# Performance work log

Measured on AMD Instinct MI355X. Metric: run time of the kernel, lower is better.

Reference implementation:

```python
import jax, jax.numpy as jnp
import numpy as np

CH = 512      # input channels
V = 320       # codewords per group
G = 2         # groups
CV_DIM = 256  # codevector_dim (wav2vec2 default)
D = CV_DIM // G
TAU = 2.0     # gumbel temperature


def setup_inputs() -> dict:
    key = jax.random.key(0)
    k1, k2, k3, k4 = jax.random.split(key, 4)
    B, T = 32, 1024
    x = jax.random.normal(k1, (B, T, CH), jnp.float32)
    W_proj = jax.random.normal(k2, (CH, G * V), jnp.float32) / np.sqrt(CH)
    b_proj = jnp.zeros((G * V,), jnp.float32)
    codevectors = jax.random.normal(k3, (G, V, D), jnp.float32) * 0.02
    # uniform noise, transformed to Gumbel inside reference
    u_noise = jax.random.uniform(k4, (B, T, G, V), jnp.float32,
                                 minval=1e-6, maxval=1.0 - 1e-6)
    return {"x": x, "W_proj": W_proj, "b_proj": b_proj,
            "codevectors": codevectors, "u_noise": u_noise}


def reference(x, W_proj, b_proj, codevectors, u_noise):
    B, T, _ = x.shape
    # projection to per-group logits: [B,T,G,V]
    logits = (x @ W_proj + b_proj).reshape(B, T, G, V)
    # gumbel-softmax (hard, straight-through)
    g = -jnp.log(-jnp.log(u_noise))
    soft = jax.nn.softmax((logits + g) / TAU, axis=-1)
    hard = jax.nn.one_hot(jnp.argmax(soft, axis=-1), V, dtype=soft.dtype)
    st = hard + soft - jax.lax.stop_gradient(soft)
    # combine selected codewords per group, concat groups -> [B,T,CV_DIM]
    out = jnp.einsum('btgv,gvd->btgd', st, codevectors).reshape(B, T, G * D)
    return out
```

## Files before the change

kernel.cpp:

```cpp
#include <hip/hip_runtime.h>
#include <cmath>

namespace {

typedef _Float16 half8 __attribute__((ext_vector_type(8)));
typedef _Float16 half4v __attribute__((ext_vector_type(4)));
typedef float f32x4 __attribute__((ext_vector_type(4)));

constexpr int M_TOTAL = 32 * 1024;
constexpr int K_CH    = 512;
constexpr int NV      = 640;
constexpr int D_CV    = 128;
constexpr int NSLOT   = 10;

constexpr int BM = 128, BN = 128, BK = 32;
constexpr int NTILE  = NV / BN;
constexpr int NPANEL = M_TOTAL / BM;
constexpr int NBLK   = NTILE * NPANEL;
constexpr int KT     = K_CH / BK;

constexpr float LO_SCALE = 4096.0f;
constexpr float LO_INV   = 1.0f / 4096.0f;

__device__ __forceinline__ void gld16(const void* g, void* l) {
  __builtin_amdgcn_global_load_lds(
      (__attribute__((address_space(1))) void*)g,
      (__attribute__((address_space(3))) void*)l, 16, 0, 0);
}

__global__ __launch_bounds__(256)
void prep_w(const float* __restrict__ W, _Float16* __restrict__ Wth,
            _Float16* __restrict__ Wtl)
{
  __shared__ float tile[32][33];
  const int bk = blockIdx.x & 15;
  const int bn = blockIdx.x >> 4;
  const int k0 = bk * 32, n0 = bn * 32;
  const int t = threadIdx.x;
  const int nn = t & 31, kk = t >> 5;
  #pragma unroll
  for (int p = 0; p < 4; ++p)
    tile[kk + p * 8][nn] = W[(size_t)(k0 + kk + p * 8) * NV + n0 + nn];
  __syncthreads();
  const int kx = t & 31, nx = t >> 5;
  #pragma unroll
  for (int p = 0; p < 4; ++p) {
    const float v = tile[kx][nx + p * 8];
    const _Float16 h = (_Float16)v;
    const _Float16 l = (_Float16)((v - (float)h) * LO_SCALE);
    const size_t o = (size_t)(n0 + nx + p * 8) * K_CH + k0 + kx;
    Wth[o] = h;
    Wtl[o] = l;
  }
}

__global__ __launch_bounds__(256)
void prep_x(const float* __restrict__ x, _Float16* __restrict__ Xh,
            _Float16* __restrict__ Xl)
{
  const size_t i = ((size_t)blockIdx.x * 256 + threadIdx.x) * 2;
  #pragma unroll
  for (int j = 0; j < 2; ++j) {
    const float4 v = reinterpret_cast<const float4*>(x)[i + j];
    const float* pv = &v.x;
    half4v h, l;
    #pragma unroll
    for (int e = 0; e < 4; ++e) {
      const _Float16 hh = (_Float16)pv[e];
      h[e] = hh;
      l[e] = (_Float16)((pv[e] - (float)hh) * LO_SCALE);
    }
    reinterpret_cast<half4v*>(Xh)[i + j] = h;
    reinterpret_cast<half4v*>(Xl)[i + j] = l;
  }
}

__global__ __launch_bounds__(256, 2)
void gvq_mfma5(const _Float16* __restrict__ Xh, const _Float16* __restrict__ Xl,
               const _Float16* __restrict__ Wth, const _Float16* __restrict__ Wtl,
               const float* __restrict__ bias, const float* __restrict__ u,
               float* __restrict__ pval, int* __restrict__ pidx)
{
  __shared__ __align__(16) _Float16 lds[2][16384];

  const int chunk = NBLK / 8;
  const int nid   = (blockIdx.x % 8) * chunk + blockIdx.x / 8;
  const int panel = nid / NTILE, ntile = nid % NTILE;
  const int m0 = panel * BM, n0 = ntile * BN;

  const int t    = threadIdx.x;
  const int wv   = t >> 6, lane = t & 63;
  const int wr   = wv >> 1, wc = wv & 1;
  const int li   = lane & 15, q = lane >> 4;

  const int r0 = t >> 2;
  const int gc = (t & 3) ^ ((t >> 3) & 3);
  const _Float16* pxh0 = Xh  + (size_t)(m0 + r0) * K_CH + gc * 8;
  const _Float16* pxh1 = Xh  + (size_t)(m0 + 64 + r0) * K_CH + gc * 8;
  const _Float16* pxl0 = Xl  + (size_t)(m0 + r0) * K_CH + gc * 8;
  const _Float16* pxl1 = Xl  + (size_t)(m0 + 64 + r0) * K_CH + gc * 8;
  const _Float16* pbh0 = Wth + (size_t)(n0 + r0) * K_CH + gc * 8;
  const _Float16* pbh1 = Wth + (size_t)(n0 + 64 + r0) * K_CH + gc * 8;
  const _Float16* pbl0 = Wtl + (size_t)(n0 + r0) * K_CH + gc * 8;
  const _Float16* pbl1 = Wtl + (size_t)(n0 + 64 + r0) * K_CH + gc * 8;

  f32x4 acc1[4][4];
  f32x4 acc2[4][4];
  #pragma unroll
  for (int i = 0; i < 4; ++i)
    #pragma unroll
    for (int j = 0; j < 4; ++j) {
      acc1[i][j] = (f32x4){0.f, 0.f, 0.f, 0.f};
      acc2[i][j] = (f32x4){0.f, 0.f, 0.f, 0.f};
    }

  auto stage = [&](int kt, int b) {
    const int ko = kt * BK;
    _Float16* L = &lds[b][0];
    gld16(pxh0 + ko, L + 0     + wv * 512);
    gld16(pxh1 + ko, L + 2048  + wv * 512);
    gld16(pxl0 + ko, L + 4096  + wv * 512);
    gld16(pxl1 + ko, L + 6144  + wv * 512);
    gld16(pbh0 + ko, L + 8192  + wv * 512);
    gld16(pbh1 + ko, L + 10240 + wv * 512);
    gld16(pbl0 + ko, L + 12288 + wv * 512);
    gld16(pbl1 + ko, L + 14336 + wv * 512);
  };

  const int soff = ((q ^ ((li >> 1) & 3)) << 3);
  const int arow = (wr * 64 + li) * 32;
  const int brow = (wc * 64 + li) * 32;

  stage(0, 0);
  stage(1, 1);
  #pragma unroll
  for (int kt = 0; kt < KT; ++kt) {
    const int cur = kt & 1;
    if (kt < KT - 1) asm volatile("s_waitcnt vmcnt(8)" ::: "memory");
    else             asm volatile("s_waitcnt vmcnt(0)" ::: "memory");
    __builtin_amdgcn_s_barrier();

    const _Float16* L = &lds[cur][0];
    half8 ah[4], al[4], bh[4], bl[4];
    #pragma unroll
    for (int f = 0; f < 4; ++f) {
      ah[f] = *reinterpret_cast<const half8*>(L + arow + f * 512 + soff);
      al[f] = *reinterpret_cast<const half8*>(L + 4096  + arow + f * 512 + soff);
      bh[f] = *reinterpret_cast<const half8*>(L + 8192  + brow + f * 512 + soff);
      bl[f] = *reinterpret_cast<const half8*>(L + 12288 + brow + f * 512 + soff);
    }
    asm volatile("s_waitcnt lgkmcnt(0)" ::: "memory");
    __builtin_amdgcn_sched_barrier(0);
    __builtin_amdgcn_s_barrier();

    if (kt + 2 < KT) stage(kt + 2, cur);

    __builtin_amdgcn_s_setprio(1);
    #pragma unroll
    for (int fm = 0; fm < 4; ++fm)
      #pragma unroll
      for (int fn = 0; fn < 4; ++fn) {
        acc1[fm][fn] = __builtin_amdgcn_mfma_f32_16x16x32_f16(
            ah[fm], bh[fn], acc1[fm][fn], 0, 0, 0);
        acc2[fm][fn] = __builtin_amdgcn_mfma_f32_16x16x32_f16(
            ah[fm], bl[fn], acc2[fm][fn], 0, 0, 0);
        acc2[fm][fn] = __builtin_amdgcn_mfma_f32_16x16x32_f16(
            al[fm], bh[fn], acc2[fm][fn], 0, 0, 0);
      }
    __builtin_amdgcn_s_setprio(0);
  }

  const int colbase = n0 + wc * 64 + li;
  float bb[4];
  #pragma unroll
  for (int fn = 0; fn < 4; ++fn) bb[fn] = bias[colbase + fn * 16];

  const int slot = ntile * 2 + wc;
  #pragma unroll
  for (int fm = 0; fm < 4; ++fm) {
    #pragma unroll
    for (int r = 0; r < 4; ++r) {
      const int m = m0 + wr * 64 + fm * 16 + q * 4 + r;
      float bv = -INFINITY;
      int   bi = 0x7fffffff;
      #pragma unroll
      for (int fn = 0; fn < 4; ++fn) {
        const float uu  = u[(size_t)m * NV + colbase + fn * 16];
        const float g   = -__logf(-__logf(uu));
        const float val = acc1[fm][fn][r] + acc2[fm][fn][r] * LO_INV
                          + bb[fn] + g;
        const int   n   = colbase + fn * 16;
        if (val > bv) { bv = val; bi = n; }
      }
      #pragma unroll
      for (int s = 1; s <= 8; s <<= 1) {
        const float ov = __shfl_xor(bv, s);
        const int   oi = __shfl_xor(bi, s);
        if (ov > bv || (ov == bv && oi < bi)) { bv = ov; bi = oi; }
      }
      if (li == 0) {
        pval[(size_t)m * NSLOT + slot] = bv;
        pidx[(size_t)m * NSLOT + slot] = bi;
      }
    }
  }
}

__global__ __launch_bounds__(256)
void gvq_gather(const float* __restrict__ pval,
                const int*   __restrict__ pidx,
                const float* __restrict__ cv,
                float* __restrict__ out)
{
  const int tid  = threadIdx.x;
  const int w    = tid >> 6;
  const int lane = tid & 63;
  const int m    = blockIdx.x * 4 + w;
  const int g    = lane >> 5;

  const float* pv = &pval[(size_t)m * NSLOT + g * 5];
  const int*   pi = &pidx[(size_t)m * NSLOT + g * 5];
  float bv = pv[0];
  int   bi = pi[0];
  #pragma unroll
  for (int s = 1; s < 5; ++s) {
    const float v = pv[s];
    const int   i = pi[s];
    if (v > bv || (v == bv && i < bi)) { bv = v; bi = i; }
  }
  const float4 src = *reinterpret_cast<const float4*>(
      &cv[(size_t)bi * D_CV + (lane & 31) * 4]);
  *reinterpret_cast<float4*>(&out[(size_t)m * 256 + lane * 4]) = src;
}

}

extern "C" void kernel_launch(void* const* d_in, const int* in_sizes, int n_in,
                              void* d_out, int out_size, void* d_ws, size_t ws_size,
                              hipStream_t stream)
{
  const float* x    = (const float*)d_in[0];
  const float* W    = (const float*)d_in[1];
  const float* bias = (const float*)d_in[2];
  const float* cv   = (const float*)d_in[3];
  const float* u    = (const float*)d_in[4];
  float* out = (float*)d_out;

  _Float16* Wth  = (_Float16*)d_ws;
  _Float16* Wtl  = Wth + (size_t)NV * K_CH;
  float*    pval = (float*)(Wtl + (size_t)NV * K_CH);
  int*      pidx = (int*)(pval + (size_t)M_TOTAL * NSLOT);
  _Float16* Xh   = (_Float16*)(pidx + (size_t)M_TOTAL * NSLOT);
  _Float16* Xl   = Xh + (size_t)M_TOTAL * K_CH;

  hipLaunchKernelGGL(prep_w, dim3(320), dim3(256), 0, stream, W, Wth, Wtl);
  hipLaunchKernelGGL(prep_x, dim3(8192), dim3(256), 0, stream, x, Xh, Xl);
  hipLaunchKernelGGL(gvq_mfma5, dim3(NBLK), dim3(256), 0, stream,
                     Xh, Xl, Wth, Wtl, bias, u, pval, pidx);
  hipLaunchKernelGGL(gvq_gather, dim3(M_TOTAL / 4), dim3(256), 0, stream,
                     pval, pidx, cv, out);
}
```

Measured before the change: 132.7 us.

## Shrink GEMM N-tile to 64, re-split waves along M, single-stage prefetch

Halves the block tile width from 128 to 64 columns, so each of the four waves now owns 32 rows by all 64 columns instead of a 2x2 wave grid. LDS per block drops, launch bounds move to 3 blocks per CU, and the pipeline becomes prefetch-next-then-compute with a full vmcnt(0) wait and barrier per k-step. Each block now writes one argmax slot per tile rather than two. The goal is higher occupancy and fewer per-wave accumulators, at the cost of reloading the X panel twice as often across N tiles and less latency hiding per block.

Result: slower. 137.2 us (+3.4%).

```diff
diff --git a/kernel.cpp b/kernel.cpp
--- a/kernel.cpp
+++ b/kernel.cpp
@@ -13,11 +13,13 @@
 constexpr int D_CV    = 128;
 constexpr int NSLOT   = 10;
 
-constexpr int BM = 128, BN = 128, BK = 32;
+constexpr int BM = 128, BN = 64, BK = 32;
 constexpr int NTILE  = NV / BN;
 constexpr int NPANEL = M_TOTAL / BM;
 constexpr int NBLK   = NTILE * NPANEL;
 constexpr int KT     = K_CH / BK;
+
+constexpr int LBUF = 12288;
 
 constexpr float LO_SCALE = 4096.0f;
 constexpr float LO_INV   = 1.0f / 4096.0f;
@@ -75,13 +77,13 @@
   }
 }
 
-__global__ __launch_bounds__(256, 2)
-void gvq_mfma5(const _Float16* __restrict__ Xh, const _Float16* __restrict__ Xl,
+__global__ __launch_bounds__(256, 3)
+void gvq_mfma6(const _Float16* __restrict__ Xh, const _Float16* __restrict__ Xl,
                const _Float16* __restrict__ Wth, const _Float16* __restrict__ Wtl,
                const float* __restrict__ bias, const float* __restrict__ u,
                float* __restrict__ pval, int* __restrict__ pidx)
 {
-  __shared__ __align__(16) _Float16 lds[2][16384];
+  __shared__ __align__(16) _Float16 lds[2 * LBUF];
 
   const int chunk = NBLK / 8;
   const int nid   = (blockIdx.x % 8) * chunk + blockIdx.x / 8;
@@ -90,24 +92,19 @@
 
   const int t    = threadIdx.x;
   const int wv   = t >> 6, lane = t & 63;
-  const int wr   = wv >> 1, wc = wv & 1;
   const int li   = lane & 15, q = lane >> 4;
 
   const int r0 = t >> 2;
   const int gc = (t & 3) ^ ((t >> 3) & 3);
-  const _Float16* pxh0 = Xh  + (size_t)(m0 + r0) * K_CH + gc * 8;
-  const _Float16* pxh1 = Xh  + (size_t)(m0 + 64 + r0) * K_CH + gc * 8;
-  const _Float16* pxl0 = Xl  + (size_t)(m0 + r0) * K_CH + gc * 8;
-  const _Float16* pxl1 = Xl  + (size_t)(m0 + 64 + r0) * K_CH + gc * 8;
-  const _Float16* pbh0 = Wth + (size_t)(n0 + r0) * K_CH + gc * 8;
-  const _Float16* pbh1 = Wth + (size_t)(n0 + 64 + r0) * K_CH + gc * 8;
-  const _Float16* pbl0 = Wtl + (size_t)(n0 + r0) * K_CH + gc * 8;
-  const _Float16* pbl1 = Wtl + (size_t)(n0 + 64 + r0) * K_CH + gc * 8;
-
-  f32x4 acc1[4][4];
-  f32x4 acc2[4][4];
-  #pragma unroll
-  for (int i = 0; i < 4; ++i)
+  const _Float16* pxh = Xh  + (size_t)(m0 + r0) * K_CH + gc * 8;
+  const _Float16* pxl = Xl  + (size_t)(m0 + r0) * K_CH + gc * 8;
+  const _Float16* pbh = Wth + (size_t)(n0 + r0) * K_CH + gc * 8;
+  const _Float16* pbl = Wtl + (size_t)(n0 + r0) * K_CH + gc * 8;
+
+  f32x4 acc1[2][4];
+  f32x4 acc2[2][4];
+  #pragma unroll
+  for (int i = 0; i < 2; ++i)
     #pragma unroll
     for (int j = 0; j < 4; ++j) {
       acc1[i][j] = (f32x4){0.f, 0.f, 0.f, 0.f};
@@ -116,48 +113,44 @@
 
   auto stage = [&](int kt, int b) {
     const int ko = kt * BK;
-    _Float16* L = &lds[b][0];
-    gld16(pxh0 + ko, L + 0     + wv * 512);
-    gld16(pxh1 + ko, L + 2048  + wv * 512);
-    gld16(pxl0 + ko, L + 4096  + wv * 512);
-    gld16(pxl1 + ko, L + 6144  + wv * 512);
-    gld16(pbh0 + ko, L + 8192  + wv * 512);
-    gld16(pbh1 + ko, L + 10240 + wv * 512);
-    gld16(pbl0 + ko, L + 12288 + wv * 512);
-    gld16(pbl1 + ko, L + 14336 + wv * 512);
+    _Float16* L = &lds[b * LBUF];
+    gld16(pxh + ko,                      L + 0     + wv * 512);
+    gld16(pxh + (size_t)64 * K_CH + ko,  L + 2048  + wv * 512);
+    gld16(pxl + ko,                      L + 4096  + wv * 512);
+    gld16(pxl + (size_t)64 * K_CH + ko,  L + 6144  + wv * 512);
+    gld16(pbh + ko,                      L + 8192  + wv * 512);
+    gld16(pbl + ko,                      L + 10240 + wv * 512);
   };
 
   const int soff = ((q ^ ((li >> 1) & 3)) << 3);
-  const int arow = (wr * 64 + li) * 32;
-  const int brow = (wc * 64 + li) * 32;
+  const int arow = (wv * 32 + li) * 32;
+  const int brow = li * 32;
 
   stage(0, 0);
-  stage(1, 1);
+  asm volatile("s_waitcnt vmcnt(0)" ::: "memory");
+  __builtin_amdgcn_s_barrier();
+  __builtin_amdgcn_sched_barrier(0);
+
   #pragma unroll
   for (int kt = 0; kt < KT; ++kt) {
     const int cur = kt & 1;
-    if (kt < KT - 1) asm volatile("s_waitcnt vmcnt(8)" ::: "memory");
-    else             asm volatile("s_waitcnt vmcnt(0)" ::: "memory");
-    __builtin_amdgcn_s_barrier();
-
-    const _Float16* L = &lds[cur][0];
-    half8 ah[4], al[4], bh[4], bl[4];
-    #pragma unroll
-    for (int f = 0; f < 4; ++f) {
-      ah[f] = *reinterpret_cast<const half8*>(L + arow + f * 512 + soff);
-      al[f] = *reinterpret_cast<const half8*>(L + 4096  + arow + f * 512 + soff);
-      bh[f] = *reinterpret_cast<const half8*>(L + 8192  + brow + f * 512 + soff);
-      bl[f] = *reinterpret_cast<const half8*>(L + 12288 + brow + f * 512 + soff);
-    }
-    asm volatile("s_waitcnt lgkmcnt(0)" ::: "memory");
-    __builtin_amdgcn_sched_barrier(0);
-    __builtin_amdgcn_s_barrier();
-
-    if (kt + 2 < KT) stage(kt + 2, cur);
-
+    if (kt + 1 < KT) stage(kt + 1, cur ^ 1);
+
+    const _Float16* L = &lds[cur * LBUF];
+    half8 bh[4], bl[4], ah[2], al[2];
+    #pragma unroll
+    for (int fn = 0; fn < 4; ++fn) {
+      bh[fn] = *reinterpret_cast<const half8*>(L + 8192  + brow + fn * 512 + soff);
+      bl[fn] = *reinterpret_cast<const half8*>(L + 10240 + brow + fn * 512 + soff);
+    }
+    #pragma unroll
+    for (int fm = 0; fm < 2; ++fm) {
+      ah[fm] = *reinterpret_cast<const half8*>(L + arow + fm * 512 + soff);
+      al[fm] = *reinterpret_cast<const half8*>(L + 4096 + arow + fm * 512 + soff);
+    }
     __builtin_amdgcn_s_setprio(1);
     #pragma unroll
-    for (int fm = 0; fm < 4; ++fm)
+    for (int fm = 0; fm < 2; ++fm)
       #pragma unroll
       for (int fn = 0; fn < 4; ++fn) {
         acc1[fm][fn] = __builtin_amdgcn_mfma_f32_16x16x32_f16(
@@ -168,19 +161,25 @@
             al[fm], bh[fn], acc2[fm][fn], 0, 0, 0);
       }
     __builtin_amdgcn_s_setprio(0);
-  }
-
-  const int colbase = n0 + wc * 64 + li;
+
+    if (kt + 1 < KT) {
+      asm volatile("s_waitcnt vmcnt(0)" ::: "memory");
+      __builtin_amdgcn_s_barrier();
+      __builtin_amdgcn_sched_barrier(0);
+    }
+  }
+
+  const int colbase = n0 + li;
   float bb[4];
   #pragma unroll
   for (int fn = 0; fn < 4; ++fn) bb[fn] = bias[colbase + fn * 16];
 
-  const int slot = ntile * 2 + wc;
-  #pragma unroll
-  for (int fm = 0; fm < 4; ++fm) {
+  const int slot = ntile;
+  #pragma unroll
+  for (int fm = 0; fm < 2; ++fm) {
     #pragma unroll
     for (int r = 0; r < 4; ++r) {
-      const int m = m0 + wr * 64 + fm * 16 + q * 4 + r;
+      const int m = m0 + wv * 32 + fm * 16 + q * 4 + r;
       float bv = -INFINITY;
       int   bi = 0x7fffffff;
       #pragma unroll
@@ -255,7 +254,7 @@
 
   hipLaunchKernelGGL(prep_w, dim3(320), dim3(256), 0, stream, W, Wth, Wtl);
   hipLaunchKernelGGL(prep_x, dim3(8192), dim3(256), 0, stream, x, Xh, Xl);
-  hipLaunchKernelGGL(gvq_mfma5, dim3(NBLK), dim3(256), 0, stream,
+  hipLaunchKernelGGL(gvq_mfma6, dim3(NBLK), dim3(256), 0, stream,
                      Xh, Xl, Wth, Wtl, bias, u, pval, pidx);
   hipLaunchKernelGGL(gvq_gather, dim3(M_TOTAL / 4), dim3(256), 0, stream,
                      pval, pidx, cv, out);
```

## Replace LDS staging with direct global-to-register fragment loads in split-fp16 GEMM

Applied to the files above, without the earlier changes.

Removes the shared-memory double buffer and the barriers in the GEMM main loop. Each wave now loads its MFMA A and B fragments straight from global memory into registers, using a software pipeline that alternates even and odd k-steps. The goal is to cut LDS traffic and barrier stalls. The cost is that every wave re-reads tiles other waves also use, relying on L1/L2 instead of LDS reuse, and issues less coalesced 16-byte row loads.

Result: slower. 209.2 us (+57.6%).

```diff
diff --git a/kernel.cpp b/kernel.cpp
--- a/kernel.cpp
+++ b/kernel.cpp
@@ -21,12 +21,6 @@
 
 constexpr float LO_SCALE = 4096.0f;
 constexpr float LO_INV   = 1.0f / 4096.0f;
-
-__device__ __forceinline__ void gld16(const void* g, void* l) {
-  __builtin_amdgcn_global_load_lds(
-      (__attribute__((address_space(1))) void*)g,
-      (__attribute__((address_space(3))) void*)l, 16, 0, 0);
-}
 
 __global__ __launch_bounds__(256)
 void prep_w(const float* __restrict__ W, _Float16* __restrict__ Wth,
@@ -76,13 +70,11 @@
 }
 
 __global__ __launch_bounds__(256, 2)
-void gvq_mfma5(const _Float16* __restrict__ Xh, const _Float16* __restrict__ Xl,
+void gvq_mfma8(const _Float16* __restrict__ Xh, const _Float16* __restrict__ Xl,
                const _Float16* __restrict__ Wth, const _Float16* __restrict__ Wtl,
                const float* __restrict__ bias, const float* __restrict__ u,
                float* __restrict__ pval, int* __restrict__ pidx)
 {
-  __shared__ __align__(16) _Float16 lds[2][16384];
-
   const int chunk = NBLK / 8;
   const int nid   = (blockIdx.x % 8) * chunk + blockIdx.x / 8;
   const int panel = nid / NTILE, ntile = nid % NTILE;
@@ -93,16 +85,10 @@
   const int wr   = wv >> 1, wc = wv & 1;
   const int li   = lane & 15, q = lane >> 4;
 
-  const int r0 = t >> 2;
-  const int gc = (t & 3) ^ ((t >> 3) & 3);
-  const _Float16* pxh0 = Xh  + (size_t)(m0 + r0) * K_CH + gc * 8;
-  const _Float16* pxh1 = Xh  + (size_t)(m0 + 64 + r0) * K_CH + gc * 8;
-  const _Float16* pxl0 = Xl  + (size_t)(m0 + r0) * K_CH + gc * 8;
-  const _Float16* pxl1 = Xl  + (size_t)(m0 + 64 + r0) * K_CH + gc * 8;
-  const _Float16* pbh0 = Wth + (size_t)(n0 + r0) * K_CH + gc * 8;
-  const _Float16* pbh1 = Wth + (size_t)(n0 + 64 + r0) * K_CH + gc * 8;
-  const _Float16* pbl0 = Wtl + (size_t)(n0 + r0) * K_CH + gc * 8;
-  const _Float16* pbl1 = Wtl + (size_t)(n0 + 64 + r0) * K_CH + gc * 8;
+  const _Float16* pAh = Xh  + (size_t)(m0 + wr * 64 + li) * K_CH + q * 8;
+  const _Float16* pAl = Xl  + (size_t)(m0 + wr * 64 + li) * K_CH + q * 8;
+  const _Float16* pBh = Wth + (size_t)(n0 + wc * 64 + li) * K_CH + q * 8;
+  const _Float16* pBl = Wtl + (size_t)(n0 + wc * 64 + li) * K_CH + q * 8;
 
   f32x4 acc1[4][4];
   f32x4 acc2[4][4];
@@ -114,60 +100,60 @@
       acc2[i][j] = (f32x4){0.f, 0.f, 0.f, 0.f};
     }
 
-  auto stage = [&](int kt, int b) {
+  half8 ahE[4], alE[4], ahO[4], alO[4];
+  half8 bh0, bl0, bh1, bl1;
+
+  auto loadA = [&](int kt, half8* ah, half8* al) {
     const int ko = kt * BK;
-    _Float16* L = &lds[b][0];
-    gld16(pxh0 + ko, L + 0     + wv * 512);
-    gld16(pxh1 + ko, L + 2048  + wv * 512);
-    gld16(pxl0 + ko, L + 4096  + wv * 512);
-    gld16(pxl1 + ko, L + 6144  + wv * 512);
-    gld16(pbh0 + ko, L + 8192  + wv * 512);
-    gld16(pbh1 + ko, L + 10240 + wv * 512);
-    gld16(pbl0 + ko, L + 12288 + wv * 512);
-    gld16(pbl1 + ko, L + 14336 + wv * 512);
+    #pragma unroll
+    for (int f = 0; f < 4; ++f) {
+      ah[f] = *reinterpret_cast<const half8*>(pAh + (size_t)f * 16 * K_CH + ko);
+      al[f] = *reinterpret_cast<const half8*>(pAl + (size_t)f * 16 * K_CH + ko);
+    }
   };
-
-  const int soff = ((q ^ ((li >> 1) & 3)) << 3);
-  const int arow = (wr * 64 + li) * 32;
-  const int brow = (wc * 64 + li) * 32;
-
-  stage(0, 0);
-  stage(1, 1);
-  #pragma unroll
-  for (int kt = 0; kt < KT; ++kt) {
-    const int cur = kt & 1;
-    if (kt < KT - 1) asm volatile("s_waitcnt vmcnt(8)" ::: "memory");
-    else             asm volatile("s_waitcnt vmcnt(0)" ::: "memory");
-    __builtin_amdgcn_s_barrier();
-
-    const _Float16* L = &lds[cur][0];
-    half8 ah[4], al[4], bh[4], bl[4];
-    #pragma unroll
-    for (int f = 0; f < 4; ++f) {
-      ah[f] = *reinterpret_cast<const half8*>(L + arow + f * 512 + soff);
-      al[f] = *reinterpret_cast<const half8*>(L + 4096  + arow + f * 512 + soff);
-      bh[f] = *reinterpret_cast<const half8*>(L + 8192  + brow + f * 512 + soff);
-      bl[f] = *reinterpret_cast<const half8*>(L + 12288 + brow + f * 512 + soff);
-    }
-    asm volatile("s_waitcnt lgkmcnt(0)" ::: "memory");
-    __builtin_amdgcn_sched_barrier(0);
-    __builtin_amdgcn_s_barrier();
-
-    if (kt + 2 < KT) stage(kt + 2, cur);
-
+  auto loadB = [&](int kt, int fn, half8& bh, half8& bl) {
+    const int ko = kt * BK;
+    bh = *reinterpret_cast<const half8*>(pBh + (size_t)fn * 16 * K_CH + ko);
+    bl = *reinterpret_cast<const half8*>(pBl + (size_t)fn * 16 * K_CH + ko);
+  };
+  auto mfmaFN = [&](int fn, half8* ah, half8* al, half8 bh, half8 bl) {
     __builtin_amdgcn_s_setprio(1);
     #pragma unroll
-    for (int fm = 0; fm < 4; ++fm)
-      #pragma unroll
-      for (int fn = 0; fn < 4; ++fn) {
-        acc1[fm][fn] = __builtin_amdgcn_mfma_f32_16x16x32_f16(
-            ah[fm], bh[fn], acc1[fm][fn], 0, 0, 0);
-        acc2[fm][fn] = __builtin_amdgcn_mfma_f32_16x16x32_f16(
-            ah[fm], bl[fn], acc2[fm][fn], 0, 0, 0);
-        acc2[fm][fn] = __builtin_amdgcn_mfma_f32_16x16x32_f16(
-            al[fm], bh[fn], acc2[fm][fn], 0, 0, 0);
-      }
+    for (int fm = 0; fm < 4; ++fm) {
+      acc1[fm][fn] = __builtin_amdgcn_mfma_f32_16x16x32_f16(
+          ah[fm], bh, acc1[fm][fn], 0, 0, 0);
+      acc2[fm][fn] = __builtin_amdgcn_mfma_f32_16x16x32_f16(
+          ah[fm], bl, acc2[fm][fn], 0, 0, 0);
+      acc2[fm][fn] = __builtin_amdgcn_mfma_f32_16x16x32_f16(
+          al[fm], bh, acc2[fm][fn], 0, 0, 0);
+    }
     __builtin_amdgcn_s_setprio(0);
+  };
+
+  loadA(0, ahE, alE);
+  loadB(0, 0, bh0, bl0);
+
+  #pragma unroll
+  for (int kt = 0; kt < KT; kt += 2) {
+    loadB(kt, 1, bh1, bl1);
+    loadA(kt + 1, ahO, alO);
+    mfmaFN(0, ahE, alE, bh0, bl0);
+    loadB(kt, 2, bh0, bl0);
+    mfmaFN(1, ahE, alE, bh1, bl1);
+    loadB(kt, 3, bh1, bl1);
+    mfmaFN(2, ahE, alE, bh0, bl0);
+    loadB(kt + 1, 0, bh0, bl0);
+    mfmaFN(3, ahE, alE, bh1, bl1);
+
+    loadB(kt + 1, 1, bh1, bl1);
+    if (kt + 2 < KT) loadA(kt + 2, ahE, alE);
+    mfmaFN(0, ahO, alO, bh0, bl0);
+    loadB(kt + 1, 2, bh0, bl0);
+    mfmaFN(1, ahO, alO, bh1, bl1);
+    loadB(kt + 1, 3, bh1, bl1);
+    mfmaFN(2, ahO, alO, bh0, bl0);
+    if (kt + 2 < KT) loadB(kt + 2, 0, bh0, bl0);
+    mfmaFN(3, ahO, alO, bh1, bl1);
   }
 
   const int colbase = n0 + wc * 64 + li;
@@ -255,7 +241,7 @@
 
   hipLaunchKernelGGL(prep_w, dim3(320), dim3(256), 0, stream, W, Wth, Wtl);
   hipLaunchKernelGGL(prep_x, dim3(8192), dim3(256), 0, stream, x, Xh, Xl);
-  hipLaunchKernelGGL(gvq_mfma5, dim3(NBLK), dim3(256), 0, stream,
+  hipLaunchKernelGGL(gvq_mfma8, dim3(NBLK), dim3(256), 0, stream,
                      Xh, Xl, Wth, Wtl, bias, u, pval, pidx);
   hipLaunchKernelGGL(gvq_gather, dim3(M_TOTAL / 4), dim3(256), 0, stream,
                      pval, pidx, cv, out);
```
